# Kernel optimization log

Measured on AMD Instinct MI355X. Metric: run time of the kernel, lower is better.

## Reference

```python
import jax, jax.numpy as jnp
import numpy as np
import math

HIDDEN = 256
NUM_GAUSSIANS = 64
NUM_FILTERS = 256
CUTOFF = 1.0
COSINE_OFFSET = 0.0
N_NODES = 10000
N_EDGES = 320000


def ssp(x):
    # shifted softplus: softplus(x) - log(2)
    return jax.nn.softplus(x) - jnp.log(2.0).astype(x.dtype)


def setup_inputs() -> dict:
    key = jax.random.key(0)
    ks = jax.random.split(key, 12)

    def xavier(k, fan_out, fan_in):
        a = math.sqrt(6.0 / (fan_in + fan_out))
        return jax.random.uniform(k, (fan_out, fan_in), jnp.float32, -a, a)

    x = jax.random.normal(ks[0], (N_NODES, HIDDEN), jnp.float32)
    ji_pairs = jax.random.randint(ks[1], (2, N_EDGES), 0, N_NODES, jnp.int64)
    e_ji = jax.random.uniform(ks[2], (N_EDGES,), jnp.float32)  # distances in [0, cutoff)
    e_ji_basis = jax.random.normal(ks[3], (N_EDGES, NUM_GAUSSIANS), jnp.float32)

    return {
        "x": x,
        "ji_pairs": ji_pairs,
        "e_ji": e_ji,
        "e_ji_basis": e_ji_basis,
        # filter_nn: Linear(G->F), ssp, Linear(F->F)
        "fw1": xavier(ks[4], NUM_FILTERS, NUM_GAUSSIANS),
        "fb1": jnp.zeros((NUM_FILTERS,), jnp.float32),
        "fw2": xavier(ks[5], NUM_FILTERS, NUM_FILTERS),
        "fb2": jnp.zeros((NUM_FILTERS,), jnp.float32),
        # CFConv linears
        "w1": xavier(ks[6], NUM_FILTERS, HIDDEN),            # linear1, no bias
        "w2": xavier(ks[7], HIDDEN, NUM_FILTERS),            # linear2
        "b2": jnp.zeros((HIDDEN,), jnp.float32),
        # linear3
        "w3": xavier(ks[8], HIDDEN, HIDDEN),
        "b3": jnp.zeros((HIDDEN,), jnp.float32),
    }


def reference(x, ji_pairs, e_ji, e_ji_basis, fw1, fb1, fw2, fb2, w1, w2, b2, w3, b3):
    pi = jnp.asarray(math.pi, x.dtype)
    # cosine cutoff: C = 0.25 * (cos((e - off) * pi / (cutoff - off)) + 1)
    C = 0.25 * (jnp.cos((e_ji - COSINE_OFFSET) * pi / (CUTOFF - COSINE_OFFSET)) + 1.0)
    # filter network on edge RBF features: [E, F]
    W = ssp(e_ji_basis @ fw1.T + fb1) @ fw2.T + fb2
    W = W * C[:, None]
    # linear1 (no bias): [N, F]
    h = x @ w1.T
    # message: x_j * W, gathered from source nodes ji_pairs[0]
    src, dst = ji_pairs[0], ji_pairs[1]
    msg = h[src] * W                                   # [E, F]
    agg = jax.ops.segment_sum(msg, dst, num_segments=x.shape[0])  # [N, F]
    # linear2
    out = agg @ w2.T + b2
    # interaction block tail: act + linear3
    out = ssp(out) @ w3.T + b3
    return out
```

## Files before the change

kernel.cpp:

```cpp
#include <hip/hip_runtime.h>
#include <hip/hip_bf16.h>

typedef __bf16 bf16_t;
typedef float f32x4 __attribute__((ext_vector_type(4)));
typedef __bf16 bf16x8 __attribute__((ext_vector_type(8)));

#define NNODES 10000
#define NEDGES 320000
#define NPAD   10048
#define NPB    8
#define NBLK   (NPAD / NPB)

#define OFF_AGG   256
#define OFF_JIN   (OFF_AGG  + (size_t)NPAD * 256 * 4)
#define OFF_HIST  (OFF_JIN  + (size_t)2 * NEDGES * 4)
#define OFF_CUR   (OFF_HIST + 10240 * 4)
#define OFF_CSR   (OFF_CUR  + 10240 * 4)
#define OFF_PERM  (OFF_CSR  + 10240 * 4)
#define OFF_SRCS  (OFF_PERM + (size_t)NEDGES * 4)
#define OFF_DSTS  (OFF_SRCS + (size_t)NEDGES * 4)
#define OFF_CES   (OFF_DSTS + (size_t)NEDGES * 4)
#define OFF_CE    (OFF_CES  + (size_t)NEDGES * 4)
#define OFF_WB    (OFF_CE   + (size_t)NEDGES * 4)
#define FW1B 0
#define FW2B 16384
#define W1B  81920
#define W2B  147456
#define W3B  212992
#define FB1B 278528
#define FB2B 278784
#define B2B  279040
#define B3B  279296
#define WBN  279552
#define WS_NEED (OFF_WB + (size_t)WBN * 2)

__device__ __forceinline__ float ssp_f(float v) {
    return fmaxf(v, 0.f) + __logf(1.f + __expf(-fabsf(v))) - 0.69314718055994531f;
}
__device__ __forceinline__ f32x4 mfma16(bf16x8 a, bf16x8 b, f32x4 c) {
    return __builtin_amdgcn_mfma_f32_16x16x32_bf16(a, b, c, 0, 0, 0);
}
template<bool ISB>
__device__ __forceinline__ bf16x8 ld8(const void* p, size_t off) {
    if constexpr (ISB) return *(const bf16x8*)((const bf16_t*)p + off);
    else {
        const float* f = (const float*)p + off;
        f32x4 lo = *(const f32x4*)f, hi = *(const f32x4*)(f + 4);
        bf16x8 r;
        for (int j = 0; j < 4; ++j) { r[j] = (bf16_t)lo[j]; r[j + 4] = (bf16_t)hi[j]; }
        return r;
    }
}
template<bool ISB>
__device__ __forceinline__ void st1(void* p, size_t off, float v) {
    if constexpr (ISB) ((bf16_t*)p)[off] = (bf16_t)v;
    else               ((float*)p)[off] = v;
}
__device__ __forceinline__ float ld1r(bool isb, const void* p, size_t off) {
    return isb ? (float)((const bf16_t*)p)[off] : ((const float*)p)[off];
}

__global__ __launch_bounds__(256) void detect_kernel(
    const void* __restrict__ x, const int* __restrict__ jraw, int* __restrict__ flags)
{
    __shared__ int cnt, hi;
    if (threadIdx.x == 0) { cnt = 0; hi = 0; }
    __syncthreads();
    const unsigned short* xw = (const unsigned short*)x;
    int local = 0;
    for (int i = threadIdx.x; i < 2048; i += 256) {
        unsigned int e = (xw[2 * i] >> 7) & 0xFF;
        if (e >= 100 && e <= 141) local++;
    }
    atomicAdd(&cnt, local);
    int v = 0;
    for (int i = threadIdx.x; i < 1024; i += 256) v |= jraw[2 * i + 1];
    if (v != 0) atomicOr(&hi, 1);
    __syncthreads();
    if (threadIdx.x == 0) { flags[0] = (cnt > 1024) ? 1 : 0; flags[1] = (hi == 0) ? 1 : 0; }
}

__global__ __launch_bounds__(256) void prep_kernel(
    const int* __restrict__ raw, const int* __restrict__ flags,
    const void* __restrict__ e_ji,
    const void* fw1, const void* fb1, const void* fw2, const void* fb2,
    const void* w1, const void* w2, const void* b2, const void* w3, const void* b3,
    int* __restrict__ jin, int* __restrict__ hist, float* __restrict__ ce,
    bf16_t* __restrict__ wb)
{
    const bool is64 = (flags[1] != 0);
    const bool isb  = (flags[0] != 0);
    const int gid = blockIdx.x * 256 + threadIdx.x;
    if (gid < 2 * NEDGES) {
        int iv = is64 ? raw[2 * gid] : raw[gid];
        iv = iv < 0 ? 0 : (iv >= NNODES ? NNODES - 1 : iv);
        jin[gid] = iv;
    }
    if (gid < NEDGES)
        ce[gid] = 0.25f * (cosf(3.14159265358979f * ld1r(isb, e_ji, gid)) + 1.0f);
    if (gid < 10240) hist[gid] = 0;
    if (gid < WBN) {
        int g = gid; const void* s; int so;
        if      (g < FW2B) { s = fw1; so = g - FW1B; }
        else if (g < W1B)  { s = fw2; so = g - FW2B; }
        else if (g < W2B)  { s = w1;  so = g - W1B; }
        else if (g < W3B)  { s = w2;  so = g - W2B; }
        else if (g < FB1B) { s = w3;  so = g - W3B; }
        else if (g < FB2B) { s = fb1; so = g - FB1B; }
        else if (g < B2B)  { s = fb2; so = g - FB2B; }
        else if (g < B3B)  { s = b2;  so = g - B2B; }
        else               { s = b3;  so = g - B3B; }
        wb[gid] = (bf16_t)ld1r(isb, s, so);
    }
}

__global__ __launch_bounds__(256) void hist_kernel(
    const int* __restrict__ jin, int* __restrict__ hist)
{
    int e = blockIdx.x * 256 + threadIdx.x;
    if (e < NEDGES) atomicAdd(&hist[jin[NEDGES + e]], 1);
}

__global__ __launch_bounds__(256) void scan_kernel(
    const int* __restrict__ hist, int* __restrict__ cur, int* __restrict__ csr)
{
    __shared__ int s[256];
    const int t = threadIdx.x;
    int loc[40]; int sum = 0;
    const int base = t * 40;
    for (int j = 0; j < 40; ++j) {
        int i = base + j;
        loc[j] = (i < NNODES) ? hist[i] : 0;
        sum += loc[j];
    }
    s[t] = sum; __syncthreads();
    for (int off = 1; off < 256; off <<= 1) {
        int v = (t >= off) ? s[t - off] : 0;
        __syncthreads();
        if (t >= off) s[t] += v;
        __syncthreads();
    }
    int pre = (t == 0) ? 0 : s[t - 1];
    for (int j = 0; j < 40; ++j) {
        int i = base + j;
        cur[i] = pre;
        csr[i] = pre;
        pre += loc[j];
    }
}

__global__ __launch_bounds__(256) void scatter_kernel(
    const int* __restrict__ jin, const float* __restrict__ ce,
    int* __restrict__ cur, int* __restrict__ perm,
    int* __restrict__ src_s, int* __restrict__ dst_s, float* __restrict__ ce_s)
{
    int e = blockIdx.x * 256 + threadIdx.x;
    if (e < NEDGES) {
        int d = jin[NEDGES + e];
        int pos = atomicAdd(&cur[d], 1);
        perm[pos]  = e;
        src_s[pos] = jin[e];
        dst_s[pos] = d;
        ce_s[pos]  = ce[e];
    }
}

template<bool ISB>
__global__ __launch_bounds__(256, 2) void h_gemm_kernel(
    const void* __restrict__ x, const bf16_t* __restrict__ wb,
    bf16_t* __restrict__ h, const int* __restrict__ flags)
{
    if ((flags[0] != 0) != ISB) return;
    const bf16_t* w1b = wb + W1B;
    const int w = threadIdx.x >> 6, L = threadIdx.x & 63;
    const int lane16 = L & 15, quad = L >> 4;
    const int nb = blockIdx.x * 64, cb = w * 64;
    f32x4 acc[4][4] = {};
    for (int kc = 0; kc < 8; ++kc) {
        const int ko = kc * 32 + quad * 8;
        bf16x8 af[4], bfr[4];
        for (int mt = 0; mt < 4; ++mt) {
            int row = nb + mt * 16 + lane16;
            if (row >= NNODES) row = NNODES - 1;
            af[mt] = ld8<ISB>(x, (size_t)row * 256 + ko);
        }
        for (int nt = 0; nt < 4; ++nt)
            bfr[nt] = *(const bf16x8*)(w1b + (size_t)(cb + nt * 16 + lane16) * 256 + ko);
        for (int mt = 0; mt < 4; ++mt)
            for (int nt = 0; nt < 4; ++nt)
                acc[mt][nt] = mfma16(af[mt], bfr[nt], acc[mt][nt]);
    }
    for (int mt = 0; mt < 4; ++mt)
        for (int r = 0; r < 4; ++r) {
            int row = nb + mt * 16 + quad * 4 + r;
            if (row < NNODES)
                for (int nt = 0; nt < 4; ++nt)
                    h[(size_t)row * 256 + cb + nt * 16 + lane16] = (bf16_t)acc[mt][nt][r];
        }
}

template<bool ISB>
__global__ __launch_bounds__(256, 3) void edge_kernel(
    const void* __restrict__ basis, const int* __restrict__ csr,
    const int* __restrict__ perm, const int* __restrict__ src_s,
    const int* __restrict__ dst_s, const float* __restrict__ ce_s,
    const bf16_t* __restrict__ wb, const bf16_t* __restrict__ h,
    float* __restrict__ agg, const int* __restrict__ flags)
{
    if ((flags[0] != 0) != ISB) return;
    __shared__ bf16_t T[64][264];
    __shared__ float G[NPB][260];
    __shared__ int sperm[64], ssrc[64], snrow[64];
    __shared__ float sce[64];
    const int tid = threadIdx.x;
    const int w = tid >> 6, L = tid & 63;
    const int lane16 = L & 15, quad = L >> 4;
    const int cb = w * 64;
    const int nbase  = blockIdx.x * NPB;
    const int estart = csr[nbase];
    const int eend   = csr[nbase + NPB];

    for (int i = tid; i < NPB * 260; i += 256) (&G[0][0])[i] = 0.f;

    const bf16_t* fw1b = wb + FW1B;
    const bf16_t* fw2b = wb + FW2B;
    float fb1v[4], fb2v[4];
    for (int nt = 0; nt < 4; ++nt) {
        fb1v[nt] = (float)wb[FB1B + cb + nt * 16 + lane16];
        fb2v[nt] = (float)wb[FB2B + cb + nt * 16 + lane16];
    }

    for (int e0 = estart & ~63; e0 < eend; e0 += 64) {
        __syncthreads();
        if (tid < 64) {
            int e = e0 + tid;
            bool valid = (e >= estart) && (e < eend);
            int ee = valid ? e : estart;
            sperm[tid] = perm[ee];
            ssrc[tid]  = src_s[ee];
            int nr = dst_s[ee] - nbase;
            nr = nr < 0 ? 0 : (nr > NPB - 1 ? NPB - 1 : nr);
            snrow[tid] = nr;
            sce[tid]   = valid ? ce_s[ee] : 0.f;
        }
        __syncthreads();

        int prow[4];
        for (int mt = 0; mt < 4; ++mt) prow[mt] = sperm[mt * 16 + lane16];

        f32x4 acc1[4][4] = {};
        for (int kc = 0; kc < 2; ++kc) {
            const int ko = kc * 32 + quad * 8;
            bf16x8 af[4], bfr[4];
            for (int mt = 0; mt < 4; ++mt)
                af[mt] = ld8<ISB>(basis, (size_t)prow[mt] * 64 + ko);
            for (int nt = 0; nt < 4; ++nt)
                bfr[nt] = *(const bf16x8*)(fw1b + (size_t)(cb + nt * 16 + lane16) * 64 + ko);
            for (int mt = 0; mt < 4; ++mt)
                for (int nt = 0; nt < 4; ++nt)
                    acc1[mt][nt] = mfma16(af[mt], bfr[nt], acc1[mt][nt]);
        }
        for (int nt = 0; nt < 4; ++nt) {
            int col = cb + nt * 16 + lane16;
            for (int mt = 0; mt < 4; ++mt)
                for (int r = 0; r < 4; ++r)
                    T[mt * 16 + quad * 4 + r][col] = (bf16_t)ssp_f(acc1[mt][nt][r] + fb1v[nt]);
        }
        __syncthreads();

        f32x4 acc2[4][4] = {};
        for (int kc = 0; kc < 8; ++kc) {
            const int ko = kc * 32 + quad * 8;
            bf16x8 af[4], bfr[4];
            for (int mt = 0; mt < 4; ++mt)
                af[mt] = *(const bf16x8*)(&T[mt * 16 + lane16][ko]);
            for (int nt = 0; nt < 4; ++nt)
                bfr[nt] = *(const bf16x8*)(fw2b + (size_t)(cb + nt * 16 + lane16) * 256 + ko);
            for (int mt = 0; mt < 4; ++mt)
                for (int nt = 0; nt < 4; ++nt)
                    acc2[mt][nt] = mfma16(af[mt], bfr[nt], acc2[mt][nt]);
        }
        __syncthreads();

        {
            const int row = tid >> 2, seg = tid & 3;
            const bf16_t* src = h + (size_t)ssrc[row] * 256 + seg * 64;
            bf16_t* dst = &T[row][seg * 64];
            #pragma unroll
            for (int j = 0; j < 8; ++j)
                ((bf16x8*)dst)[j] = ((const bf16x8*)src)[j];
        }
        __syncthreads();

        float run[4] = {0, 0, 0, 0};
        int curn = -1;
        for (int mt = 0; mt < 4; ++mt)
            for (int r = 0; r < 4; ++r) {
                int row = mt * 16 + quad * 4 + r;
                int nr = snrow[row];
                if (nr != curn) {
                    if (curn >= 0)
                        for (int nt = 0; nt < 4; ++nt)
                            atomicAdd(&G[curn][cb + nt * 16 + lane16], run[nt]);
                    curn = nr;
                    run[0] = run[1] = run[2] = run[3] = 0.f;
                }
                float cv = sce[row];
                for (int nt = 0; nt < 4; ++nt) {
                    int col = cb + nt * 16 + lane16;
                    run[nt] += (acc2[mt][nt][r] + fb2v[nt]) * cv * (float)T[row][col];
                }
            }
        if (curn >= 0)
            for (int nt = 0; nt < 4; ++nt)
                atomicAdd(&G[curn][cb + nt * 16 + lane16], run[nt]);
    }
    __syncthreads();

    for (int n = 0; n < NPB; ++n)
        agg[(size_t)(nbase + n) * 256 + tid] = G[n][tid];
}

template<bool ISB>
__global__ __launch_bounds__(256, 2) void out_kernel(
    const float* __restrict__ agg, const bf16_t* __restrict__ wb,
    void* __restrict__ out, const int* __restrict__ flags)
{
    if ((flags[0] != 0) != ISB) return;
    const bf16_t* w2b = wb + W2B;
    const bf16_t* w3b = wb + W3B;
    __shared__ bf16_t U[64][264];
    const int w = threadIdx.x >> 6, L = threadIdx.x & 63;
    const int lane16 = L & 15, quad = L >> 4;
    const int nb = blockIdx.x * 64, cb = w * 64;

    f32x4 acc[4][4] = {};
    for (int kc = 0; kc < 8; ++kc) {
        const int ko = kc * 32 + quad * 8;
        bf16x8 af[4], bfr[4];
        for (int mt = 0; mt < 4; ++mt) {
            int row = nb + mt * 16 + lane16;
            const float* p = agg + (size_t)row * 256 + ko;
            f32x4 lo = *(const f32x4*)p, hi = *(const f32x4*)(p + 4);
            bf16x8 a;
            for (int j = 0; j < 4; ++j) { a[j] = (bf16_t)lo[j]; a[j + 4] = (bf16_t)hi[j]; }
            af[mt] = a;
        }
        for (int nt = 0; nt < 4; ++nt)
            bfr[nt] = *(const bf16x8*)(w2b + (size_t)(cb + nt * 16 + lane16) * 256 + ko);
        for (int mt = 0; mt < 4; ++mt)
            for (int nt = 0; nt < 4; ++nt)
                acc[mt][nt] = mfma16(af[mt], bfr[nt], acc[mt][nt]);
    }
    for (int nt = 0; nt < 4; ++nt) {
        int col = cb + nt * 16 + lane16;
        float bias = (float)wb[B2B + col];
        for (int mt = 0; mt < 4; ++mt)
            for (int r = 0; r < 4; ++r)
                U[mt * 16 + quad * 4 + r][col] = (bf16_t)ssp_f(acc[mt][nt][r] + bias);
    }
    __syncthreads();

    f32x4 acc2[4][4] = {};
    for (int kc = 0; kc < 8; ++kc) {
        const int ko = kc * 32 + quad * 8;
        bf16x8 af[4], bfr[4];
        for (int mt = 0; mt < 4; ++mt)
            af[mt] = *(const bf16x8*)(&U[mt * 16 + lane16][ko]);
        for (int nt = 0; nt < 4; ++nt)
            bfr[nt] = *(const bf16x8*)(w3b + (size_t)(cb + nt * 16 + lane16) * 256 + ko);
        for (int mt = 0; mt < 4; ++mt)
            for (int nt = 0; nt < 4; ++nt)
                acc2[mt][nt] = mfma16(af[mt], bfr[nt], acc2[mt][nt]);
    }
    for (int mt = 0; mt < 4; ++mt)
        for (int r = 0; r < 4; ++r) {
            int row = nb + mt * 16 + quad * 4 + r;
            if (row < NNODES)
                for (int nt = 0; nt < 4; ++nt) {
                    int col = cb + nt * 16 + lane16;
                    st1<ISB>(out, (size_t)row * 256 + col,
                             acc2[mt][nt][r] + (float)wb[B3B + col]);
                }
        }
}

extern "C" void kernel_launch(void* const* d_in, const int* in_sizes, int n_in,
                              void* d_out, int out_size, void* d_ws, size_t ws_size,
                              hipStream_t stream) {
    const void* x     = d_in[0];
    const int*  ji    = (const int*)d_in[1];
    const void* e_ji  = d_in[2];
    const void* basis = d_in[3];
    const void* fw1   = d_in[4];
    const void* fb1   = d_in[5];
    const void* fw2   = d_in[6];
    const void* fb2   = d_in[7];
    const void* w1    = d_in[8];
    const void* w2    = d_in[9];
    const void* b2    = d_in[10];
    const void* w3    = d_in[11];
    const void* b3    = d_in[12];

    if (ws_size < WS_NEED) return;

    char* W = (char*)d_ws;
    int*    flags = (int*)W;
    float*  agg   = (float*)(W + OFF_AGG);
    int*    jin   = (int*)(W + OFF_JIN);
    int*    hist  = (int*)(W + OFF_HIST);
    int*    cur   = (int*)(W + OFF_CUR);
    int*    csr   = (int*)(W + OFF_CSR);
    int*    perm  = (int*)(W + OFF_PERM);
    int*    src_s = (int*)(W + OFF_SRCS);
    int*    dst_s = (int*)(W + OFF_DSTS);
    float*  ce_s  = (float*)(W + OFF_CES);
    float*  ce    = (float*)(W + OFF_CE);
    bf16_t* wb    = (bf16_t*)(W + OFF_WB);
    bf16_t* h     = (bf16_t*)d_out;

    detect_kernel<<<1, 256, 0, stream>>>(x, ji, flags);
    prep_kernel<<<2500, 256, 0, stream>>>(ji, flags, e_ji, fw1, fb1, fw2, fb2,
                                          w1, w2, b2, w3, b3, jin, hist, ce, wb);
    hist_kernel<<<1250, 256, 0, stream>>>(jin, hist);
    scan_kernel<<<1, 256, 0, stream>>>(hist, cur, csr);
    scatter_kernel<<<1250, 256, 0, stream>>>(jin, ce, cur, perm, src_s, dst_s, ce_s);
    h_gemm_kernel<true ><<<157, 256, 0, stream>>>(x, wb, h, flags);
    h_gemm_kernel<false><<<157, 256, 0, stream>>>(x, wb, h, flags);
    edge_kernel<true ><<<NBLK, 256, 0, stream>>>(basis, csr, perm, src_s, dst_s, ce_s, wb, h, agg, flags);
    edge_kernel<false><<<NBLK, 256, 0, stream>>>(basis, csr, perm, src_s, dst_s, ce_s, wb, h, agg, flags);
    out_kernel<true ><<<157, 256, 0, stream>>>(agg, wb, d_out, flags);
    out_kernel<false><<<157, 256, 0, stream>>>(agg, wb, d_out, flags);
}
```

Baseline: 607.3 us.

## Pre-convert basis to bf16, fuse histogram into prep, prefetch h rows

```diff
diff --git a/kernel.cpp b/kernel.cpp
--- a/kernel.cpp
+++ b/kernel.cpp
@@ -33,6 +33,8 @@
 #define B3B  279296
 #define WBN  279552
 #define WS_NEED (OFF_WB + (size_t)WBN * 2)
+#define OFF_BASC  ((WS_NEED + 255) & ~(size_t)255)
+#define WS_NEED_BIG (OFF_BASC + (size_t)NEDGES * 64 * 2)
 
 __device__ __forceinline__ float ssp_f(float v) {
     return fmaxf(v, 0.f) + __logf(1.f + __expf(-fabsf(v))) - 0.69314718055994531f;
@@ -51,6 +53,14 @@
         return r;
     }
 }
+__device__ __forceinline__ bf16x8 ld8r(bool isb, const void* p, size_t off) {
+    if (isb) return *(const bf16x8*)((const bf16_t*)p + off);
+    const float* f = (const float*)p + off;
+    f32x4 lo = *(const f32x4*)f, hi = *(const f32x4*)(f + 4);
+    bf16x8 r;
+    for (int j = 0; j < 4; ++j) { r[j] = (bf16_t)lo[j]; r[j + 4] = (bf16_t)hi[j]; }
+    return r;
+}
 template<bool ISB>
 __device__ __forceinline__ void st1(void* p, size_t off, float v) {
     if constexpr (ISB) ((bf16_t*)p)[off] = (bf16_t)v;
@@ -61,7 +71,8 @@
 }
 
 __global__ __launch_bounds__(256) void detect_kernel(
-    const void* __restrict__ x, const int* __restrict__ jraw, int* __restrict__ flags)
+    const void* __restrict__ x, const int* __restrict__ jraw,
+    int* __restrict__ flags, int* __restrict__ hist)
 {
     __shared__ int cnt, hi;
     if (threadIdx.x == 0) { cnt = 0; hi = 0; }
@@ -76,17 +87,18 @@
     int v = 0;
     for (int i = threadIdx.x; i < 1024; i += 256) v |= jraw[2 * i + 1];
     if (v != 0) atomicOr(&hi, 1);
+    for (int i = threadIdx.x; i < 10240; i += 256) hist[i] = 0;
     __syncthreads();
     if (threadIdx.x == 0) { flags[0] = (cnt > 1024) ? 1 : 0; flags[1] = (hi == 0) ? 1 : 0; }
 }
 
 __global__ __launch_bounds__(256) void prep_kernel(
     const int* __restrict__ raw, const int* __restrict__ flags,
-    const void* __restrict__ e_ji,
+    const void* __restrict__ e_ji, const void* __restrict__ basis,
     const void* fw1, const void* fb1, const void* fw2, const void* fb2,
     const void* w1, const void* w2, const void* b2, const void* w3, const void* b3,
     int* __restrict__ jin, int* __restrict__ hist, float* __restrict__ ce,
-    bf16_t* __restrict__ wb)
+    bf16_t* __restrict__ wb, bf16_t* __restrict__ basc, int doconv)
 {
     const bool is64 = (flags[1] != 0);
     const bool isb  = (flags[0] != 0);
@@ -95,10 +107,10 @@
         int iv = is64 ? raw[2 * gid] : raw[gid];
         iv = iv < 0 ? 0 : (iv >= NNODES ? NNODES - 1 : iv);
         jin[gid] = iv;
+        if (gid >= NEDGES) atomicAdd(&hist[iv], 1);
     }
     if (gid < NEDGES)
         ce[gid] = 0.25f * (cosf(3.14159265358979f * ld1r(isb, e_ji, gid)) + 1.0f);
-    if (gid < 10240) hist[gid] = 0;
     if (gid < WBN) {
         int g = gid; const void* s; int so;
         if      (g < FW2B) { s = fw1; so = g - FW1B; }
@@ -112,13 +124,11 @@
         else               { s = b3;  so = g - B3B; }
         wb[gid] = (bf16_t)ld1r(isb, s, so);
     }
-}
-
-__global__ __launch_bounds__(256) void hist_kernel(
-    const int* __restrict__ jin, int* __restrict__ hist)
-{
-    int e = blockIdx.x * 256 + threadIdx.x;
-    if (e < NEDGES) atomicAdd(&hist[jin[NEDGES + e]], 1);
+    if (doconv) {
+        const int nv = NEDGES * 64 / 8;
+        for (int i = gid; i < nv; i += gridDim.x * 256)
+            ((bf16x8*)basc)[i] = ld8r(isb, basis, (size_t)i * 8);
+    }
 }
 
 __global__ __launch_bounds__(256) void scan_kernel(
@@ -199,7 +209,7 @@
         }
 }
 
-template<bool ISB>
+template<bool ISB, bool CONV>
 __global__ __launch_bounds__(256, 3) void edge_kernel(
     const void* __restrict__ basis, const int* __restrict__ csr,
     const int* __restrict__ perm, const int* __restrict__ src_s,
@@ -207,7 +217,7 @@
     const bf16_t* __restrict__ wb, const bf16_t* __restrict__ h,
     float* __restrict__ agg, const int* __restrict__ flags)
 {
-    if ((flags[0] != 0) != ISB) return;
+    if (!CONV && (flags[0] != 0) != ISB) return;
     __shared__ bf16_t T[64][264];
     __shared__ float G[NPB][260];
     __shared__ int sperm[64], ssrc[64], snrow[64];
@@ -230,20 +240,31 @@
         fb2v[nt] = (float)wb[FB2B + cb + nt * 16 + lane16];
     }
 
+    const int hrow = tid >> 2, hseg = tid & 3;
+
     for (int e0 = estart & ~63; e0 < eend; e0 += 64) {
         __syncthreads();
-        if (tid < 64) {
-            int e = e0 + tid;
+        {
+            int g = tid >> 6, i = tid & 63;
+            int e = e0 + i;
             bool valid = (e >= estart) && (e < eend);
             int ee = valid ? e : estart;
-            sperm[tid] = perm[ee];
-            ssrc[tid]  = src_s[ee];
-            int nr = dst_s[ee] - nbase;
-            nr = nr < 0 ? 0 : (nr > NPB - 1 ? NPB - 1 : nr);
-            snrow[tid] = nr;
-            sce[tid]   = valid ? ce_s[ee] : 0.f;
-        }
-        __syncthreads();
+            if      (g == 0) sperm[i] = perm[ee];
+            else if (g == 1) ssrc[i] = src_s[ee];
+            else if (g == 2) {
+                int nr = dst_s[ee] - nbase;
+                snrow[i] = nr < 0 ? 0 : (nr > NPB - 1 ? NPB - 1 : nr);
+            }
+            else sce[i] = valid ? ce_s[ee] : 0.f;
+        }
+        __syncthreads();
+
+        bf16x8 hreg[8];
+        {
+            const bf16_t* hs = h + (size_t)ssrc[hrow] * 256 + hseg * 64;
+            #pragma unroll
+            for (int j = 0; j < 8; ++j) hreg[j] = ((const bf16x8*)hs)[j];
+        }
 
         int prow[4];
         for (int mt = 0; mt < 4; ++mt) prow[mt] = sperm[mt * 16 + lane16];
@@ -253,7 +274,7 @@
             const int ko = kc * 32 + quad * 8;
             bf16x8 af[4], bfr[4];
             for (int mt = 0; mt < 4; ++mt)
-                af[mt] = ld8<ISB>(basis, (size_t)prow[mt] * 64 + ko);
+                af[mt] = ld8<CONV ? true : ISB>(basis, (size_t)prow[mt] * 64 + ko);
             for (int nt = 0; nt < 4; ++nt)
                 bfr[nt] = *(const bf16x8*)(fw1b + (size_t)(cb + nt * 16 + lane16) * 64 + ko);
             for (int mt = 0; mt < 4; ++mt)
@@ -283,12 +304,9 @@
         __syncthreads();
 
         {
-            const int row = tid >> 2, seg = tid & 3;
-            const bf16_t* src = h + (size_t)ssrc[row] * 256 + seg * 64;
-            bf16_t* dst = &T[row][seg * 64];
+            bf16_t* dp = &T[hrow][hseg * 64];
             #pragma unroll
-            for (int j = 0; j < 8; ++j)
-                ((bf16x8*)dst)[j] = ((const bf16x8*)src)[j];
+            for (int j = 0; j < 8; ++j) ((bf16x8*)dp)[j] = hreg[j];
         }
         __syncthreads();
 
@@ -403,6 +421,7 @@
     const void* b3    = d_in[12];
 
     if (ws_size < WS_NEED) return;
+    const bool bigws = ws_size >= WS_NEED_BIG;
 
     char* W = (char*)d_ws;
     int*    flags = (int*)W;
@@ -417,18 +436,23 @@
     float*  ce_s  = (float*)(W + OFF_CES);
     float*  ce    = (float*)(W + OFF_CE);
     bf16_t* wb    = (bf16_t*)(W + OFF_WB);
+    bf16_t* basc  = (bf16_t*)(W + OFF_BASC);
     bf16_t* h     = (bf16_t*)d_out;
 
-    detect_kernel<<<1, 256, 0, stream>>>(x, ji, flags);
-    prep_kernel<<<2500, 256, 0, stream>>>(ji, flags, e_ji, fw1, fb1, fw2, fb2,
-                                          w1, w2, b2, w3, b3, jin, hist, ce, wb);
-    hist_kernel<<<1250, 256, 0, stream>>>(jin, hist);
+    detect_kernel<<<1, 256, 0, stream>>>(x, ji, flags, hist);
+    prep_kernel<<<2500, 256, 0, stream>>>(ji, flags, e_ji, basis, fw1, fb1, fw2, fb2,
+                                          w1, w2, b2, w3, b3, jin, hist, ce, wb,
+                                          basc, bigws ? 1 : 0);
     scan_kernel<<<1, 256, 0, stream>>>(hist, cur, csr);
     scatter_kernel<<<1250, 256, 0, stream>>>(jin, ce, cur, perm, src_s, dst_s, ce_s);
     h_gemm_kernel<true ><<<157, 256, 0, stream>>>(x, wb, h, flags);
     h_gemm_kernel<false><<<157, 256, 0, stream>>>(x, wb, h, flags);
-    edge_kernel<true ><<<NBLK, 256, 0, stream>>>(basis, csr, perm, src_s, dst_s, ce_s, wb, h, agg, flags);
-    edge_kernel<false><<<NBLK, 256, 0, stream>>>(basis, csr, perm, src_s, dst_s, ce_s, wb, h, agg, flags);
+    if (bigws) {
+        edge_kernel<true, true><<<NBLK, 256, 0, stream>>>(basc, csr, perm, src_s, dst_s, ce_s, wb, h, agg, flags);
+    } else {
+        edge_kernel<true,  false><<<NBLK, 256, 0, stream>>>(basis, csr, perm, src_s, dst_s, ce_s, wb, h, agg, flags);
+        edge_kernel<false, false><<<NBLK, 256, 0, stream>>>(basis, csr, perm, src_s, dst_s, ce_s, wb, h, agg, flags);
+    }
     out_kernel<true ><<<157, 256, 0, stream>>>(agg, wb, d_out, flags);
     out_kernel<false><<<157, 256, 0, stream>>>(agg, wb, d_out, flags);
 }
```

Measured after the change: 582.5 us. 4.1% less time.
